# Performance work log

Measured on AMD Instinct MI355X. Metric: run time of the kernel, lower is better.

Reference implementation:

```python
import jax, jax.numpy as jnp
import numpy as np

B, T, D, H = 4, 2048, 512, 8
DH = D // H


def setup_inputs() -> dict:
    key = jax.random.key(0)
    ks = jax.random.split(key, 13)
    s = 1.0 / np.sqrt(D)
    inp = {
        "q": jax.random.normal(ks[0], (B, T, D), jnp.float32),
        "k": jax.random.normal(ks[1], (B, T, D), jnp.float32),
        "v": jax.random.normal(ks[2], (B, T, D), jnp.float32),
        # key padding mask, broadcastable to [B, H, T_q, T_k]; mostly True
        "padding_mask": jax.random.uniform(ks[3], (B, 1, 1, T)) > 0.1,
        "W_q": jax.random.normal(ks[4], (D, D), jnp.float32) * s,
        "b_q": jnp.zeros((D,), jnp.float32),
        "W_k": jax.random.normal(ks[5], (D, D), jnp.float32) * s,
        "b_k": jnp.zeros((D,), jnp.float32),
        "W_v": jax.random.normal(ks[6], (D, D), jnp.float32) * s,
        "b_v": jnp.zeros((D,), jnp.float32),
        "W_o": jax.random.normal(ks[7], (D, D), jnp.float32) * s,
        "b_o": jnp.zeros((D,), jnp.float32),
    }
    return inp


def reference(q, k, v, padding_mask, W_q, b_q, W_k, b_k, W_v, b_v, W_o, b_o):
    # Linear projections, then split heads: [B, T, D] -> [B, H, T, DH]
    def heads(x, W, b):
        y = x @ W + b
        return y.reshape(x.shape[0], x.shape[1], H, DH).transpose(0, 2, 1, 3)

    Q = heads(q, W_q, b_q)
    K = heads(k, W_k, b_k)
    V = heads(v, W_v, b_v)

    scores = jnp.einsum("bhqd,bhkd->bhqk", Q, K) / jnp.sqrt(jnp.float32(DH))
    scores = jnp.where(padding_mask, scores, -jnp.inf)
    weights = jax.nn.softmax(scores, axis=-1)
    weights = jnp.nan_to_num(weights, nan=0.0)  # all-masked rows -> 0
    x = jnp.einsum("bhqk,bhkd->bhqd", weights, V)
    x = x.transpose(0, 2, 1, 3).reshape(q.shape[0], q.shape[1], D)
    return x @ W_o + b_o
```

## Files before the change

kernel.cpp:

```cpp
#include <hip/hip_runtime.h>
#include <hip/hip_bf16.h>
#include <math.h>


#define TB 2048
#define DD 512
#define NH 8
#define DH 64

typedef short bf16x8 __attribute__((ext_vector_type(8)));
typedef float f32x4 __attribute__((ext_vector_type(4)));

static __device__ __forceinline__ ushort f2bf(float x) {
  __hip_bfloat16 h = __float2bfloat16(x);
  return *reinterpret_cast<ushort*>(&h);
}
static __device__ __forceinline__ float bf2f(ushort u) {
  unsigned int v = ((unsigned int)u) << 16;
  return __uint_as_float(v);
}
static __device__ __forceinline__ float fast_exp2(float x) {
  return __builtin_amdgcn_exp2f(x);
}
static __device__ __forceinline__ unsigned cvtpk(float lo, float hi) {
  unsigned r;
  asm("v_cvt_pk_bf16_f32 %0, %1, %2" : "=v"(r) : "v"(lo), "v"(hi));
  return r;
}
static __device__ __forceinline__ bf16x8 cvt8(float4 lo, float4 hi) {
  union { unsigned u[4]; bf16x8 v; } r;
  r.u[0] = cvtpk(lo.x, lo.y);
  r.u[1] = cvtpk(lo.z, lo.w);
  r.u[2] = cvtpk(hi.x, hi.y);
  r.u[3] = cvtpk(hi.z, hi.w);
  return r.v;
}

__global__ __launch_bounds__(256) void wtrans5_kernel(
    const float* __restrict__ Wq, const float* __restrict__ Wk,
    const float* __restrict__ Wv, const float* __restrict__ Wo,
    const unsigned char* __restrict__ pm,
    ushort* __restrict__ Wall, ushort* __restrict__ Wot,
    float* __restrict__ mbias) {
  __shared__ ushort thi[64][68];
  __shared__ ushort tlo[64][68];
  const int z = blockIdx.z;
  const int bn = blockIdx.x << 6, bk = blockIdx.y << 6;
  const int tx = threadIdx.x & 15, ty = threadIdx.x >> 4;

  if (z == 4) {
    if (blockIdx.x != 0 || blockIdx.y != 0) return;
    __shared__ int c1, c2;
    if (threadIdx.x == 0) { c1 = 0; c2 = 0; }
    __syncthreads();
    int l1 = 0, l2 = 0;
    for (int i = threadIdx.x; i < 8192; i += 256) {
      int ph = i & 3;
      unsigned char v = pm[i];
      if (ph == 1 && v) l1++;
      if (ph == 2 && v) l2++;
    }
    if (l1) atomicAdd(&c1, l1);
    if (l2) atomicAdd(&c2, l2);
    __syncthreads();
    const int md = (c1 > 0) ? 0 : ((c2 > 0) ? 1 : 2);
    for (int i = threadIdx.x; i < 8192; i += 256) {
      int v;
      if (md == 0)      v = pm[i] != 0;
      else if (md == 1) v = ((const float*)pm)[i] != 0.0f;
      else              v = ((const int*)pm)[i] != 0;
      mbias[i] = v ? -14.0f : -INFINITY;
    }
    return;
  }

  if (z < 3) {
    const float* W = (z == 0) ? Wq : (z == 1) ? Wk : Wv;
    ushort* Wt = Wall + (size_t)z * (512 * 512);
#pragma unroll
    for (int rr = 0; rr < 64; rr += 16) {
      float4 v = *(const float4*)&W[(size_t)(bk + rr + ty) * DD + bn + (tx << 2)];
      thi[(tx << 2) + 0][rr + ty] = f2bf(v.x);
      thi[(tx << 2) + 1][rr + ty] = f2bf(v.y);
      thi[(tx << 2) + 2][rr + ty] = f2bf(v.z);
      thi[(tx << 2) + 3][rr + ty] = f2bf(v.w);
    }
    __syncthreads();
#pragma unroll
    for (int rr = 0; rr < 64; rr += 16) {
      ushort4 o;
      o.x = thi[rr + ty][(tx << 2) + 0];
      o.y = thi[rr + ty][(tx << 2) + 1];
      o.z = thi[rr + ty][(tx << 2) + 2];
      o.w = thi[rr + ty][(tx << 2) + 3];
      *(ushort4*)&Wt[(size_t)(bn + rr + ty) * DD + bk + (tx << 2)] = o;
    }
  } else {
#pragma unroll
    for (int rr = 0; rr < 64; rr += 16) {
      float4 v = *(const float4*)&Wo[(size_t)(bk + rr + ty) * DD + bn + (tx << 2)];
      float vv[4] = {v.x, v.y, v.z, v.w};
#pragma unroll
      for (int c = 0; c < 4; ++c) {
        ushort hi = f2bf(vv[c]);
        ushort lo = f2bf(vv[c] - bf2f(hi));
        thi[(tx << 2) + c][rr + ty] = hi;
        tlo[(tx << 2) + c][rr + ty] = lo;
      }
    }
    __syncthreads();
#pragma unroll
    for (int rr = 0; rr < 64; rr += 16) {
      ushort4 h4, l4;
      h4.x = thi[rr + ty][(tx << 2) + 0];
      h4.y = thi[rr + ty][(tx << 2) + 1];
      h4.z = thi[rr + ty][(tx << 2) + 2];
      h4.w = thi[rr + ty][(tx << 2) + 3];
      l4.x = tlo[rr + ty][(tx << 2) + 0];
      l4.y = tlo[rr + ty][(tx << 2) + 1];
      l4.z = tlo[rr + ty][(tx << 2) + 2];
      l4.w = tlo[rr + ty][(tx << 2) + 3];
      size_t rowb = (size_t)(bn + rr + ty) * 1536;
      *(ushort4*)&Wot[rowb + bk + (tx << 2)] = h4;
      *(ushort4*)&Wot[rowb + 512 + bk + (tx << 2)] = h4;
      *(ushort4*)&Wot[rowb + 1024 + bk + (tx << 2)] = l4;
    }
  }
}

__global__ __launch_bounds__(256) void projqkv_kernel(
    const float* __restrict__ Qx, const float* __restrict__ Kx,
    const float* __restrict__ Vx, const ushort* __restrict__ Wall,
    const float* __restrict__ bq, const float* __restrict__ bk,
    const float* __restrict__ bv, ushort* __restrict__ Yall, float qscale) {
  __shared__ __align__(16) ushort As[2][128][32];
  __shared__ __align__(16) ushort Bs[2][128][32];

  const int tid = threadIdx.x;
  const int w = tid >> 6, lane = tid & 63;
  const int llo = lane & 15, lhi = lane >> 4;
  const int wm = w >> 1, wn = w & 1;

  const int bid = blockIdx.x;
  const int x = bid & 7, rest = bid >> 3;
  const int ni = rest & 3;
  const int gg = (rest >> 2) * 8 + x;
  const int sec = gg >> 6;
  const int mt = gg & 63;
  const int m0 = mt << 7;
  const int n0s = ni << 7;

  const float* A = (sec == 0) ? Qx : (sec == 1) ? Kx : Vx;
  const float* bias = (sec == 0) ? bq : (sec == 1) ? bk : bv;
  const float scale = (sec == 0) ? qscale : 1.0f;
  const ushort* Wt = Wall + (size_t)(sec * 512 + n0s) * DD;

  const int srow = tid >> 1, scol = (tid & 1) << 4;
  const float* Ag = A + (size_t)(m0 + srow) * DD + scol;
  const ushort* Bg = Wt + (size_t)srow * DD + scol;

  f32x4 acc[4][4];
#pragma unroll
  for (int mi = 0; mi < 4; ++mi)
#pragma unroll
    for (int nj = 0; nj < 4; ++nj) acc[mi][nj] = (f32x4){0.f, 0.f, 0.f, 0.f};

  {
    float4 f0 = *(const float4*)(Ag + 0);
    float4 f1 = *(const float4*)(Ag + 4);
    float4 f2 = *(const float4*)(Ag + 8);
    float4 f3 = *(const float4*)(Ag + 12);
    bf16x8 w0 = *(const bf16x8*)(Bg + 0);
    bf16x8 w1 = *(const bf16x8*)(Bg + 8);
    *(bf16x8*)&As[0][srow][scol] = cvt8(f0, f1);
    *(bf16x8*)&As[0][srow][scol + 8] = cvt8(f2, f3);
    *(bf16x8*)&Bs[0][srow][scol] = w0;
    *(bf16x8*)&Bs[0][srow][scol + 8] = w1;
  }
  __syncthreads();

  int cur = 0;
  for (int t = 0; t < 16; ++t) {
    float4 f0, f1, f2, f3;
    bf16x8 w0, w1;
    if (t < 15) {
      const float* ag = Ag + (t + 1) * 32;
      const ushort* bg = Bg + (t + 1) * 32;
      f0 = *(const float4*)(ag + 0);
      f1 = *(const float4*)(ag + 4);
      f2 = *(const float4*)(ag + 8);
      f3 = *(const float4*)(ag + 12);
      w0 = *(const bf16x8*)(bg + 0);
      w1 = *(const bf16x8*)(bg + 8);
    }
    bf16x8 af[4], bfr[4];
#pragma unroll
    for (int mi = 0; mi < 4; ++mi)
      af[mi] = *(const bf16x8*)&As[cur][wm * 64 + mi * 16 + llo][lhi * 8];
#pragma unroll
    for (int nj = 0; nj < 4; ++nj)
      bfr[nj] = *(const bf16x8*)&Bs[cur][wn * 64 + nj * 16 + llo][lhi * 8];
    __builtin_amdgcn_s_setprio(1);
#pragma unroll
    for (int mi = 0; mi < 4; ++mi)
#pragma unroll
      for (int nj = 0; nj < 4; ++nj)
        acc[mi][nj] = __builtin_amdgcn_mfma_f32_16x16x32_bf16(
            af[mi], bfr[nj], acc[mi][nj], 0, 0, 0);
    __builtin_amdgcn_s_setprio(0);
    if (t < 15) {
      *(bf16x8*)&As[cur ^ 1][srow][scol] = cvt8(f0, f1);
      *(bf16x8*)&As[cur ^ 1][srow][scol + 8] = cvt8(f2, f3);
      *(bf16x8*)&Bs[cur ^ 1][srow][scol] = w0;
      *(bf16x8*)&Bs[cur ^ 1][srow][scol + 8] = w1;
    }
    __syncthreads();
    cur ^= 1;
  }

  float bb[4];
#pragma unroll
  for (int nj = 0; nj < 4; ++nj)
    bb[nj] = bias[n0s + wn * 64 + nj * 16 + llo];

  ushort* Yq = Yall;
  ushort* Yk = Yall + ((size_t)4 << 20);
  ushort* Yv = Yall + ((size_t)8 << 20);
#pragma unroll
  for (int mi = 0; mi < 4; ++mi)
#pragma unroll
    for (int nj = 0; nj < 4; ++nj) {
      int colS = n0s + wn * 64 + nj * 16 + llo;
      int h = colS >> 6, dh = colS & (DH - 1);
#pragma unroll
      for (int r = 0; r < 4; ++r) {
        int row = m0 + wm * 64 + mi * 16 + lhi * 4 + r;
        int bidx = row >> 11, t = row & (TB - 1);
        int bh = bidx * NH + h;
        ushort u = f2bf((acc[mi][nj][r] + bb[nj]) * scale);
        if (sec == 0) {
          Yq[((size_t)(bh * 128 + (t >> 4)) * 2 + (dh >> 5)) * 512 +
             ((((dh >> 3) & 3) << 4) + (t & 15)) * 8 + (dh & 7)] = u;
        } else if (sec == 1) {
          Yk[((size_t)(bh * 32 + (t >> 6)) << 12) +
             (((dh >> 5) << 2) + ((t >> 4) & 3)) * 512 +
             ((((dh >> 3) & 3) << 4) + (t & 15)) * 8 + (dh & 7)] = u;
        } else {
          Yv[((size_t)(bh * 32 + (t >> 6)) << 12) +
             ((((t >> 5) & 1) << 2) + (dh >> 4)) * 512 +
             ((((t >> 3) & 3) << 4) + (dh & 15)) * 8 + (t & 7)] = u;
        }
      }
    }
}

__global__ __launch_bounds__(256) void projo_kernel(
    const ushort* __restrict__ A, const ushort* __restrict__ Wt,
    const float* __restrict__ bias, float* __restrict__ Y) {
  __shared__ __align__(16) ushort As[2][128][32];
  __shared__ __align__(16) ushort Bs[2][64][32];

  const int tid = threadIdx.x;
  const int w = tid >> 6, lane = tid & 63;
  const int llo = lane & 15, lhi = lane >> 4;
  const int wm = w >> 1, wn = w & 1;

  const int bid = blockIdx.x;
  const int x = bid & 7, rest = bid >> 3;
  const int ni = rest & 7;
  const int mt = (rest >> 3) * 8 + x;
  const int m0 = mt << 7;
  const int n0 = ni << 6;
  const int K = 1536;

  const int arow = tid >> 1, acol = (tid & 1) << 4;
  const int brow = tid >> 2, bcol = (tid & 3) << 3;
  const ushort* Ag = A + (size_t)(m0 + arow) * K + acol;
  const ushort* Bg = Wt + (size_t)(n0 + brow) * K + bcol;

  f32x4 acc[4][2];
#pragma unroll
  for (int mi = 0; mi < 4; ++mi)
#pragma unroll
    for (int nj = 0; nj < 2; ++nj) acc[mi][nj] = (f32x4){0.f, 0.f, 0.f, 0.f};

  {
    bf16x8 a0 = *(const bf16x8*)(Ag + 0);
    bf16x8 a1 = *(const bf16x8*)(Ag + 8);
    bf16x8 b0 = *(const bf16x8*)(Bg + 0);
    *(bf16x8*)&As[0][arow][acol] = a0;
    *(bf16x8*)&As[0][arow][acol + 8] = a1;
    *(bf16x8*)&Bs[0][brow][bcol] = b0;
  }
  __syncthreads();

  int cur = 0;
#pragma unroll 2
  for (int t = 0; t < 48; ++t) {
    bf16x8 a0, a1, b0;
    if (t < 47) {
      const ushort* ag = Ag + (t + 1) * 32;
      const ushort* bg = Bg + (t + 1) * 32;
      a0 = *(const bf16x8*)(ag + 0);
      a1 = *(const bf16x8*)(ag + 8);
      b0 = *(const bf16x8*)(bg + 0);
    }
    bf16x8 af[4], bfr[2];
#pragma unroll
    for (int mi = 0; mi < 4; ++mi)
      af[mi] = *(const bf16x8*)&As[cur][wm * 64 + mi * 16 + llo][lhi * 8];
#pragma unroll
    for (int nj = 0; nj < 2; ++nj)
      bfr[nj] = *(const bf16x8*)&Bs[cur][wn * 32 + nj * 16 + llo][lhi * 8];
    __builtin_amdgcn_s_setprio(1);
#pragma unroll
    for (int mi = 0; mi < 4; ++mi)
#pragma unroll
      for (int nj = 0; nj < 2; ++nj)
        acc[mi][nj] = __builtin_amdgcn_mfma_f32_16x16x32_bf16(
            af[mi], bfr[nj], acc[mi][nj], 0, 0, 0);
    __builtin_amdgcn_s_setprio(0);
    if (t < 47) {
      *(bf16x8*)&As[cur ^ 1][arow][acol] = a0;
      *(bf16x8*)&As[cur ^ 1][arow][acol + 8] = a1;
      *(bf16x8*)&Bs[cur ^ 1][brow][bcol] = b0;
    }
    __syncthreads();
    cur ^= 1;
  }

  float bb[2];
#pragma unroll
  for (int nj = 0; nj < 2; ++nj)
    bb[nj] = bias[n0 + wn * 32 + nj * 16 + llo];
#pragma unroll
  for (int mi = 0; mi < 4; ++mi)
#pragma unroll
    for (int nj = 0; nj < 2; ++nj) {
      int col = n0 + wn * 32 + nj * 16 + llo;
#pragma unroll
      for (int r = 0; r < 4; ++r) {
        int row = m0 + wm * 64 + mi * 16 + lhi * 4 + r;
        Y[(size_t)row * DD + col] = acc[mi][nj][r] + bb[nj];
      }
    }
}

__global__ __launch_bounds__(256) void attn_mfma_kernel(
    const ushort* __restrict__ Qf,
    const ushort* __restrict__ Kf,
    const ushort* __restrict__ Vf,
    const float* __restrict__ mbias,
    ushort* __restrict__ Ap) {
  __shared__ __align__(16) ushort Plds[4][2][16][72];

  const int tid = threadIdx.x;
  const int w = tid >> 6, lane = tid & 63;
  const int lhi = lane >> 4, llo = lane & 15;
  const int lane8 = lane * 8;

  const int bid = blockIdx.x;
  const int j = bid >> 3;
  const int bh = (bid & 7) + ((j >> 4) << 3);
  const int qt = j & 15;
  const int b = bh >> 3, h = bh & 7;
  const int q0 = qt << 7;

  const float* mb = mbias + b * TB;
  ushort* plA = &Plds[w][0][0][0];
  ushort* plB = &Plds[w][1][0][0];

  const ushort* Qb =
      Qf + ((size_t)((bh << 7) + (q0 >> 4) + w * 2) * 2) * 512 + lane8;
  bf16x8 qa0 = *(const bf16x8*)Qb;
  bf16x8 qa1 = *(const bf16x8*)(Qb + 512);
  bf16x8 qa2 = *(const bf16x8*)(Qb + 1024);
  bf16x8 qa3 = *(const bf16x8*)(Qb + 1536);

  const size_t bhK = (size_t)bh << 5;
  f32x4 oaccA[4], oaccB[4];
#pragma unroll
  for (int nt = 0; nt < 4; ++nt) {
    oaccA[nt] = (f32x4){0.f, 0.f, 0.f, 0.f};
    oaccB[nt] = (f32x4){0.f, 0.f, 0.f, 0.f};
  }
  float lA = 0.f, lB = 0.f;

  bf16x8 kf[8];
  float4 mb4[4];
  {
    const ushort* Kt0 = Kf + (bhK << 12) + lane8;
#pragma unroll
    for (int i = 0; i < 8; ++i) kf[i] = *(const bf16x8*)(Kt0 + i * 512);
#pragma unroll
    for (int nt = 0; nt < 4; ++nt)
      mb4[nt] = *(const float4*)&mb[nt * 16 + lhi * 4];
  }

  for (int kt64 = 0; kt64 < 32; ++kt64) {
    f32x4 sA[4], sB[4];
    __builtin_amdgcn_s_setprio(1);
#pragma unroll
    for (int nt = 0; nt < 4; ++nt) {
      f32x4 ci = (f32x4){mb4[nt].x, mb4[nt].y, mb4[nt].z, mb4[nt].w};
      sA[nt] = __builtin_amdgcn_mfma_f32_16x16x32_bf16(kf[nt], qa0, ci, 0, 0, 0);
      sA[nt] = __builtin_amdgcn_mfma_f32_16x16x32_bf16(kf[4 + nt], qa1, sA[nt], 0, 0, 0);
    }
#pragma unroll
    for (int nt = 0; nt < 4; ++nt) {
      f32x4 ci = (f32x4){mb4[nt].x, mb4[nt].y, mb4[nt].z, mb4[nt].w};
      sB[nt] = __builtin_amdgcn_mfma_f32_16x16x32_bf16(kf[nt], qa2, ci, 0, 0, 0);
      sB[nt] = __builtin_amdgcn_mfma_f32_16x16x32_bf16(kf[4 + nt], qa3, sB[nt], 0, 0, 0);
    }
    __builtin_amdgcn_s_setprio(0);

    const ushort* Vt = Vf + ((bhK + kt64) << 12) + lane8;
    bf16x8 vf[8];
#pragma unroll
    for (int i = 0; i < 8; ++i) vf[i] = *(const bf16x8*)(Vt + i * 512);

    {
      const int ktn = (kt64 + 1) & 31;
      const ushort* Ktn = Kf + ((bhK + ktn) << 12) + lane8;
#pragma unroll
      for (int i = 0; i < 8; ++i) kf[i] = *(const bf16x8*)(Ktn + i * 512);
#pragma unroll
      for (int nt = 0; nt < 4; ++nt)
        mb4[nt] = *(const float4*)&mb[ktn * 64 + nt * 16 + lhi * 4];
    }

#pragma unroll
    for (int nt = 0; nt < 4; ++nt)
#pragma unroll
      for (int r = 0; r < 4; ++r) {
        sA[nt][r] = fast_exp2(sA[nt][r]);
        sB[nt][r] = fast_exp2(sB[nt][r]);
      }
    {
      float a0 = (sA[0][0] + sA[0][1]) + (sA[0][2] + sA[0][3]);
      float a1 = (sA[1][0] + sA[1][1]) + (sA[1][2] + sA[1][3]);
      float a2 = (sA[2][0] + sA[2][1]) + (sA[2][2] + sA[2][3]);
      float a3 = (sA[3][0] + sA[3][1]) + (sA[3][2] + sA[3][3]);
      lA += (a0 + a1) + (a2 + a3);
      float b0 = (sB[0][0] + sB[0][1]) + (sB[0][2] + sB[0][3]);
      float b1 = (sB[1][0] + sB[1][1]) + (sB[1][2] + sB[1][3]);
      float b2 = (sB[2][0] + sB[2][1]) + (sB[2][2] + sB[2][3]);
      float b3 = (sB[3][0] + sB[3][1]) + (sB[3][2] + sB[3][3]);
      lB += (b0 + b1) + (b2 + b3);
    }

#pragma unroll
    for (int nt = 0; nt < 4; ++nt) {
      *(uint2*)&plA[llo * 72 + nt * 16 + lhi * 4] =
          make_uint2(cvtpk(sA[nt][0], sA[nt][1]), cvtpk(sA[nt][2], sA[nt][3]));
      *(uint2*)&plB[llo * 72 + nt * 16 + lhi * 4] =
          make_uint2(cvtpk(sB[nt][0], sB[nt][1]), cvtpk(sB[nt][2], sB[nt][3]));
    }

    __builtin_amdgcn_s_setprio(1);
#pragma unroll
    for (int kc = 0; kc < 2; ++kc) {
      bf16x8 paA = *(const bf16x8*)&plA[llo * 72 + kc * 32 + lhi * 8];
      bf16x8 paB = *(const bf16x8*)&plB[llo * 72 + kc * 32 + lhi * 8];
#pragma unroll
      for (int nt = 0; nt < 4; ++nt) {
        oaccA[nt] = __builtin_amdgcn_mfma_f32_16x16x32_bf16(paA, vf[kc * 4 + nt], oaccA[nt], 0, 0, 0);
        oaccB[nt] = __builtin_amdgcn_mfma_f32_16x16x32_bf16(paB, vf[kc * 4 + nt], oaccB[nt], 0, 0, 0);
      }
    }
    __builtin_amdgcn_s_setprio(0);
  }

  lA += __shfl_xor(lA, 16);
  lA += __shfl_xor(lA, 32);
  lB += __shfl_xor(lB, 16);
  lB += __shfl_xor(lB, 32);
  float invA = (lA > 0.f) ? 1.f / lA : 0.f;
  float invB = (lB > 0.f) ? 1.f / lB : 0.f;
  float ilA[4], ilB[4];
#pragma unroll
  for (int r = 0; r < 4; ++r) {
    ilA[r] = __shfl(invA, lhi * 4 + r);
    ilB[r] = __shfl(invB, lhi * 4 + r);
  }
  const int t0 = q0 + w * 32 + lhi * 4;
#pragma unroll
  for (int r = 0; r < 4; ++r) {
    size_t rowbA = (size_t)(b * TB + t0 + r) * 1536;
    size_t rowbB = (size_t)(b * TB + t0 + 16 + r) * 1536;
#pragma unroll
    for (int nt = 0; nt < 4; ++nt) {
      int c = h * DH + nt * 16 + llo;
      float oA = oaccA[nt][r] * ilA[r];
      ushort hiA = f2bf(oA);
      ushort loA = f2bf(oA - bf2f(hiA));
      Ap[rowbA + c] = hiA;
      Ap[rowbA + 512 + c] = loA;
      Ap[rowbA + 1024 + c] = hiA;
      float oB = oaccB[nt][r] * ilB[r];
      ushort hiB = f2bf(oB);
      ushort loB = f2bf(oB - bf2f(hiB));
      Ap[rowbB + c] = hiB;
      Ap[rowbB + 512 + c] = loB;
      Ap[rowbB + 1024 + c] = hiB;
    }
  }
}

extern "C" void kernel_launch(void* const* d_in, const int* in_sizes, int n_in,
                              void* d_out, int out_size, void* d_ws,
                              size_t ws_size, hipStream_t stream) {
  (void)in_sizes; (void)n_in; (void)out_size; (void)ws_size;
  const float* q = (const float*)d_in[0];
  const float* k = (const float*)d_in[1];
  const float* v = (const float*)d_in[2];
  const void* pm = d_in[3];
  const float* Wq = (const float*)d_in[4];
  const float* bq = (const float*)d_in[5];
  const float* Wk = (const float*)d_in[6];
  const float* bk = (const float*)d_in[7];
  const float* Wv = (const float*)d_in[8];
  const float* bv = (const float*)d_in[9];
  const float* Wo = (const float*)d_in[10];
  const float* bo = (const float*)d_in[11];

  char* ws = (char*)d_ws;
  const size_t MB = (size_t)1 << 20;
  ushort* Ap = (ushort*)(ws);
  ushort* Wall = (ushort*)(ws + 24 * MB);
  ushort* Wot = (ushort*)(ws + 26 * MB);
  ushort* Qh = (ushort*)(ws + 32 * MB);
  float* mbias = (float*)(ws + 56 * MB);

  wtrans5_kernel<<<dim3(8, 8, 5), 256, 0, stream>>>(
      Wq, Wk, Wv, Wo, (const unsigned char*)pm, Wall, Wot, mbias);

  const float qscale = 0.125f * 1.4426950408889634f;
  projqkv_kernel<<<768, 256, 0, stream>>>(q, k, v, Wall,
                                          bq, bk, bv, Qh, qscale);

  attn_mfma_kernel<<<512, 256, 0, stream>>>(
      Qh, Qh + ((size_t)4 << 20), Qh + ((size_t)8 << 20), mbias, Ap);

  projo_kernel<<<512, 256, 0, stream>>>(Ap, Wot, bo, (float*)d_out);
}
```

Measured before the change: 128.5 us.

## Switch attention to 32x32x16 MFMA with permlane swap instead of LDS round-trip

```diff
diff --git a/kernel.cpp b/kernel.cpp
--- a/kernel.cpp
+++ b/kernel.cpp
@@ -10,6 +10,7 @@
 
 typedef short bf16x8 __attribute__((ext_vector_type(8)));
 typedef float f32x4 __attribute__((ext_vector_type(4)));
+typedef float f32x16 __attribute__((ext_vector_type(16)));
 
 static __device__ __forceinline__ ushort f2bf(float x) {
   __hip_bfloat16 h = __float2bfloat16(x);
@@ -34,6 +35,18 @@
   r.u[2] = cvtpk(hi.x, hi.y);
   r.u[3] = cvtpk(hi.z, hi.w);
   return r.v;
+}
+static __device__ __forceinline__ void plswap(unsigned& u, unsigned& w) {
+  asm("v_permlane32_swap_b32 %0, %1" : "+v"(u), "+v"(w));
+}
+static __device__ __forceinline__ f32x16 mk16(float4 a, float4 b, float4 c,
+                                              float4 d) {
+  f32x16 r;
+  r[0] = a.x;  r[1] = a.y;  r[2] = a.z;  r[3] = a.w;
+  r[4] = b.x;  r[5] = b.y;  r[6] = b.z;  r[7] = b.w;
+  r[8] = c.x;  r[9] = c.y;  r[10] = c.z; r[11] = c.w;
+  r[12] = d.x; r[13] = d.y; r[14] = d.z; r[15] = d.w;
+  return r;
 }
 
 __global__ __launch_bounds__(256) void wtrans5_kernel(
@@ -231,24 +244,24 @@
 #pragma unroll
     for (int nj = 0; nj < 4; ++nj) {
       int colS = n0s + wn * 64 + nj * 16 + llo;
-      int h = colS >> 6, dh = colS & (DH - 1);
+      int hh = colS >> 6, dh = colS & (DH - 1);
 #pragma unroll
       for (int r = 0; r < 4; ++r) {
         int row = m0 + wm * 64 + mi * 16 + lhi * 4 + r;
         int bidx = row >> 11, t = row & (TB - 1);
-        int bh = bidx * NH + h;
+        int bh = bidx * NH + hh;
         ushort u = f2bf((acc[mi][nj][r] + bb[nj]) * scale);
-        if (sec == 0) {
-          Yq[((size_t)(bh * 128 + (t >> 4)) * 2 + (dh >> 5)) * 512 +
-             ((((dh >> 3) & 3) << 4) + (t & 15)) * 8 + (dh & 7)] = u;
-        } else if (sec == 1) {
-          Yk[((size_t)(bh * 32 + (t >> 6)) << 12) +
-             (((dh >> 5) << 2) + ((t >> 4) & 3)) * 512 +
-             ((((dh >> 3) & 3) << 4) + (t & 15)) * 8 + (dh & 7)] = u;
+        if (sec <= 1) {
+          ushort* Yb = (sec == 0) ? Yq : Yk;
+          int lane32 = ((dh >> 3) & 1) * 32 + (t & 31);
+          size_t idx = (((size_t)(bh * 64 + (t >> 5)) * 4 + (dh >> 4)) * 512) +
+                       lane32 * 8 + (dh & 7);
+          Yb[idx] = u;
         } else {
-          Yv[((size_t)(bh * 32 + (t >> 6)) << 12) +
-             ((((t >> 5) & 1) << 2) + (dh >> 4)) * 512 +
-             ((((t >> 3) & 3) << 4) + (dh & 15)) * 8 + (t & 7)] = u;
+          int lane32 = ((t >> 3) & 1) * 32 + (dh & 31);
+          size_t idx = (((size_t)(bh * 32 + (t >> 6)) * 8 + (dh >> 5) * 4 +
+                         ((t >> 4) & 3)) * 512) + lane32 * 8 + (t & 7);
+          Yv[idx] = u;
         }
       }
     }
@@ -352,157 +365,145 @@
     const ushort* __restrict__ Vf,
     const float* __restrict__ mbias,
     ushort* __restrict__ Ap) {
-  __shared__ __align__(16) ushort Plds[4][2][16][72];
-
   const int tid = threadIdx.x;
   const int w = tid >> 6, lane = tid & 63;
-  const int lhi = lane >> 4, llo = lane & 15;
+  const int h = lane >> 5;
+  const int q31 = lane & 31;
   const int lane8 = lane * 8;
 
   const int bid = blockIdx.x;
   const int j = bid >> 3;
   const int bh = (bid & 7) + ((j >> 4) << 3);
   const int qt = j & 15;
-  const int b = bh >> 3, h = bh & 7;
+  const int b = bh >> 3, hh = bh & 7;
   const int q0 = qt << 7;
 
   const float* mb = mbias + b * TB;
-  ushort* plA = &Plds[w][0][0][0];
-  ushort* plB = &Plds[w][1][0][0];
-
-  const ushort* Qb =
-      Qf + ((size_t)((bh << 7) + (q0 >> 4) + w * 2) * 2) * 512 + lane8;
-  bf16x8 qa0 = *(const bf16x8*)Qb;
-  bf16x8 qa1 = *(const bf16x8*)(Qb + 512);
-  bf16x8 qa2 = *(const bf16x8*)(Qb + 1024);
-  bf16x8 qa3 = *(const bf16x8*)(Qb + 1536);
-
-  const size_t bhK = (size_t)bh << 5;
-  f32x4 oaccA[4], oaccB[4];
-#pragma unroll
-  for (int nt = 0; nt < 4; ++nt) {
-    oaccA[nt] = (f32x4){0.f, 0.f, 0.f, 0.f};
-    oaccB[nt] = (f32x4){0.f, 0.f, 0.f, 0.f};
-  }
-  float lA = 0.f, lB = 0.f;
+
+  bf16x8 qf[4];
+  {
+    const ushort* Qb =
+        Qf + (((size_t)(bh * 64 + (q0 >> 5) + w)) << 11) + lane8;
+#pragma unroll
+    for (int c = 0; c < 4; ++c) qf[c] = *(const bf16x8*)(Qb + c * 512);
+  }
+
+  f32x16 oacc[2];
+#pragma unroll
+  for (int d = 0; d < 2; ++d)
+#pragma unroll
+    for (int r = 0; r < 16; ++r) oacc[d][r] = 0.f;
+  float l = 0.f;
 
   bf16x8 kf[8];
-  float4 mb4[4];
+  float4 mbf[8];
   {
-    const ushort* Kt0 = Kf + (bhK << 12) + lane8;
-#pragma unroll
-    for (int i = 0; i < 8; ++i) kf[i] = *(const bf16x8*)(Kt0 + i * 512);
-#pragma unroll
-    for (int nt = 0; nt < 4; ++nt)
-      mb4[nt] = *(const float4*)&mb[nt * 16 + lhi * 4];
+    const ushort* Kb = Kf + (((size_t)(bh * 64)) << 11) + lane8;
+#pragma unroll
+    for (int i = 0; i < 8; ++i) kf[i] = *(const bf16x8*)(Kb + i * 512);
+#pragma unroll
+    for (int g = 0; g < 8; ++g)
+      mbf[g] = *(const float4*)&mb[(g >> 2) * 32 + (g & 3) * 8 + 4 * h];
   }
 
   for (int kt64 = 0; kt64 < 32; ++kt64) {
-    f32x4 sA[4], sB[4];
+    f32x16 s0 = mk16(mbf[0], mbf[1], mbf[2], mbf[3]);
+    f32x16 s1 = mk16(mbf[4], mbf[5], mbf[6], mbf[7]);
     __builtin_amdgcn_s_setprio(1);
 #pragma unroll
-    for (int nt = 0; nt < 4; ++nt) {
-      f32x4 ci = (f32x4){mb4[nt].x, mb4[nt].y, mb4[nt].z, mb4[nt].w};
-      sA[nt] = __builtin_amdgcn_mfma_f32_16x16x32_bf16(kf[nt], qa0, ci, 0, 0, 0);
-      sA[nt] = __builtin_amdgcn_mfma_f32_16x16x32_bf16(kf[4 + nt], qa1, sA[nt], 0, 0, 0);
-    }
-#pragma unroll
-    for (int nt = 0; nt < 4; ++nt) {
-      f32x4 ci = (f32x4){mb4[nt].x, mb4[nt].y, mb4[nt].z, mb4[nt].w};
-      sB[nt] = __builtin_amdgcn_mfma_f32_16x16x32_bf16(kf[nt], qa2, ci, 0, 0, 0);
-      sB[nt] = __builtin_amdgcn_mfma_f32_16x16x32_bf16(kf[4 + nt], qa3, sB[nt], 0, 0, 0);
-    }
+    for (int c = 0; c < 4; ++c)
+      s0 = __builtin_amdgcn_mfma_f32_32x32x16_bf16(kf[c], qf[c], s0, 0, 0, 0);
+#pragma unroll
+    for (int c = 0; c < 4; ++c)
+      s1 = __builtin_amdgcn_mfma_f32_32x32x16_bf16(kf[4 + c], qf[c], s1, 0, 0, 0);
     __builtin_amdgcn_s_setprio(0);
 
-    const ushort* Vt = Vf + ((bhK + kt64) << 12) + lane8;
     bf16x8 vf[8];
-#pragma unroll
-    for (int i = 0; i < 8; ++i) vf[i] = *(const bf16x8*)(Vt + i * 512);
+    {
+      const ushort* Vt = Vf + (((size_t)(bh * 32 + kt64)) << 12) + lane8;
+#pragma unroll
+      for (int i = 0; i < 8; ++i) vf[i] = *(const bf16x8*)(Vt + i * 512);
+    }
 
     {
       const int ktn = (kt64 + 1) & 31;
-      const ushort* Ktn = Kf + ((bhK + ktn) << 12) + lane8;
-#pragma unroll
-      for (int i = 0; i < 8; ++i) kf[i] = *(const bf16x8*)(Ktn + i * 512);
-#pragma unroll
-      for (int nt = 0; nt < 4; ++nt)
-        mb4[nt] = *(const float4*)&mb[ktn * 64 + nt * 16 + lhi * 4];
-    }
-
-#pragma unroll
-    for (int nt = 0; nt < 4; ++nt)
-#pragma unroll
-      for (int r = 0; r < 4; ++r) {
-        sA[nt][r] = fast_exp2(sA[nt][r]);
-        sB[nt][r] = fast_exp2(sB[nt][r]);
+      const ushort* Kb = Kf + (((size_t)(bh * 64 + ktn * 2)) << 11) + lane8;
+#pragma unroll
+      for (int i = 0; i < 8; ++i) kf[i] = *(const bf16x8*)(Kb + i * 512);
+#pragma unroll
+      for (int g = 0; g < 8; ++g)
+        mbf[g] = *(const float4*)&mb[ktn * 64 + (g >> 2) * 32 + (g & 3) * 8 + 4 * h];
+    }
+
+#pragma unroll
+    for (int r = 0; r < 16; ++r) {
+      s0[r] = fast_exp2(s0[r]);
+      s1[r] = fast_exp2(s1[r]);
+    }
+    {
+      float a = (s0[0] + s0[1]) + (s0[2] + s0[3]);
+      float bb2 = (s0[4] + s0[5]) + (s0[6] + s0[7]);
+      float c = (s0[8] + s0[9]) + (s0[10] + s0[11]);
+      float d = (s0[12] + s0[13]) + (s0[14] + s0[15]);
+      float e = (s1[0] + s1[1]) + (s1[2] + s1[3]);
+      float f = (s1[4] + s1[5]) + (s1[6] + s1[7]);
+      float g = (s1[8] + s1[9]) + (s1[10] + s1[11]);
+      float i = (s1[12] + s1[13]) + (s1[14] + s1[15]);
+      l += ((a + bb2) + (c + d)) + ((e + f) + (g + i));
+    }
+
+    bf16x8 pa[4];
+    {
+      unsigned t0[8], t1[8];
+#pragma unroll
+      for (int i = 0; i < 8; ++i) {
+        t0[i] = cvtpk(s0[2 * i], s0[2 * i + 1]);
+        t1[i] = cvtpk(s1[2 * i], s1[2 * i + 1]);
       }
-    {
-      float a0 = (sA[0][0] + sA[0][1]) + (sA[0][2] + sA[0][3]);
-      float a1 = (sA[1][0] + sA[1][1]) + (sA[1][2] + sA[1][3]);
-      float a2 = (sA[2][0] + sA[2][1]) + (sA[2][2] + sA[2][3]);
-      float a3 = (sA[3][0] + sA[3][1]) + (sA[3][2] + sA[3][3]);
-      lA += (a0 + a1) + (a2 + a3);
-      float b0 = (sB[0][0] + sB[0][1]) + (sB[0][2] + sB[0][3]);
-      float b1 = (sB[1][0] + sB[1][1]) + (sB[1][2] + sB[1][3]);
-      float b2 = (sB[2][0] + sB[2][1]) + (sB[2][2] + sB[2][3]);
-      float b3 = (sB[3][0] + sB[3][1]) + (sB[3][2] + sB[3][3]);
-      lB += (b0 + b1) + (b2 + b3);
-    }
-
-#pragma unroll
-    for (int nt = 0; nt < 4; ++nt) {
-      *(uint2*)&plA[llo * 72 + nt * 16 + lhi * 4] =
-          make_uint2(cvtpk(sA[nt][0], sA[nt][1]), cvtpk(sA[nt][2], sA[nt][3]));
-      *(uint2*)&plB[llo * 72 + nt * 16 + lhi * 4] =
-          make_uint2(cvtpk(sB[nt][0], sB[nt][1]), cvtpk(sB[nt][2], sB[nt][3]));
+      plswap(t0[0], t0[2]);
+      plswap(t0[1], t0[3]);
+      plswap(t0[4], t0[6]);
+      plswap(t0[5], t0[7]);
+      plswap(t1[0], t1[2]);
+      plswap(t1[1], t1[3]);
+      plswap(t1[4], t1[6]);
+      plswap(t1[5], t1[7]);
+      union { unsigned u[4]; bf16x8 v; } p0, p1, p2, p3;
+      p0.u[0] = t0[0]; p0.u[1] = t0[1]; p0.u[2] = t0[2]; p0.u[3] = t0[3];
+      p1.u[0] = t0[4]; p1.u[1] = t0[5]; p1.u[2] = t0[6]; p1.u[3] = t0[7];
+      p2.u[0] = t1[0]; p2.u[1] = t1[1]; p2.u[2] = t1[2]; p2.u[3] = t1[3];
+      p3.u[0] = t1[4]; p3.u[1] = t1[5]; p3.u[2] = t1[6]; p3.u[3] = t1[7];
+      pa[0] = p0.v; pa[1] = p1.v; pa[2] = p2.v; pa[3] = p3.v;
     }
 
     __builtin_amdgcn_s_setprio(1);
 #pragma unroll
-    for (int kc = 0; kc < 2; ++kc) {
-      bf16x8 paA = *(const bf16x8*)&plA[llo * 72 + kc * 32 + lhi * 8];
-      bf16x8 paB = *(const bf16x8*)&plB[llo * 72 + kc * 32 + lhi * 8];
-#pragma unroll
-      for (int nt = 0; nt < 4; ++nt) {
-        oaccA[nt] = __builtin_amdgcn_mfma_f32_16x16x32_bf16(paA, vf[kc * 4 + nt], oaccA[nt], 0, 0, 0);
-        oaccB[nt] = __builtin_amdgcn_mfma_f32_16x16x32_bf16(paB, vf[kc * 4 + nt], oaccB[nt], 0, 0, 0);
-      }
-    }
+    for (int d = 0; d < 2; ++d)
+#pragma unroll
+      for (int kc = 0; kc < 4; ++kc)
+        oacc[d] = __builtin_amdgcn_mfma_f32_32x32x16_bf16(
+            pa[kc], vf[d * 4 + kc], oacc[d], 0, 0, 0);
     __builtin_amdgcn_s_setprio(0);
   }
 
-  lA += __shfl_xor(lA, 16);
-  lA += __shfl_xor(lA, 32);
-  lB += __shfl_xor(lB, 16);
-  lB += __shfl_xor(lB, 32);
-  float invA = (lA > 0.f) ? 1.f / lA : 0.f;
-  float invB = (lB > 0.f) ? 1.f / lB : 0.f;
-  float ilA[4], ilB[4];
-#pragma unroll
-  for (int r = 0; r < 4; ++r) {
-    ilA[r] = __shfl(invA, lhi * 4 + r);
-    ilB[r] = __shfl(invB, lhi * 4 + r);
-  }
-  const int t0 = q0 + w * 32 + lhi * 4;
-#pragma unroll
-  for (int r = 0; r < 4; ++r) {
-    size_t rowbA = (size_t)(b * TB + t0 + r) * 1536;
-    size_t rowbB = (size_t)(b * TB + t0 + 16 + r) * 1536;
-#pragma unroll
-    for (int nt = 0; nt < 4; ++nt) {
-      int c = h * DH + nt * 16 + llo;
-      float oA = oaccA[nt][r] * ilA[r];
-      ushort hiA = f2bf(oA);
-      ushort loA = f2bf(oA - bf2f(hiA));
-      Ap[rowbA + c] = hiA;
-      Ap[rowbA + 512 + c] = loA;
-      Ap[rowbA + 1024 + c] = hiA;
-      float oB = oaccB[nt][r] * ilB[r];
-      ushort hiB = f2bf(oB);
-      ushort loB = f2bf(oB - bf2f(hiB));
-      Ap[rowbB + c] = hiB;
-      Ap[rowbB + 512 + c] = loB;
-      Ap[rowbB + 1024 + c] = hiB;
+  l += __shfl_xor(l, 32);
+  float linv = (l > 0.f) ? 1.f / l : 0.f;
+  const int tbase = q0 + w * 32;
+#pragma unroll
+  for (int r = 0; r < 16; ++r) {
+    int kap = (r & 3) + 8 * (r >> 2);
+    float lq = __shfl(linv, kap + 4 * h);
+    int t = tbase + kap + 4 * h;
+    size_t rowb = (size_t)(b * TB + t) * 1536;
+#pragma unroll
+    for (int d = 0; d < 2; ++d) {
+      int c = hh * DH + d * 32 + q31;
+      float o = oacc[d][r] * lq;
+      ushort hi = f2bf(o);
+      ushort lo = f2bf(o - bf2f(hi));
+      Ap[rowb + c] = hi;
+      Ap[rowb + 512 + c] = lo;
+      Ap[rowb + 1024 + c] = hi;
     }
   }
 }
```

Result: slower. 137.5 us (+7.0%).
